# Performance work log

Hardware: AMD Instinct MI355X
Metric: run time of the kernel (lower is better)

The kernel has to match this reference:

```python
import jax, jax.numpy as jnp
import numpy as np

VOCAB, EMBED, ZCH = 4096, 128, 256
B, H, W = 32, 16, 16


def setup_inputs() -> dict:
    key = jax.random.key(0)
    k1, k2, k3, k4 = jax.random.split(key, 4)
    z_e = jax.random.normal(k1, (B, ZCH, H, W), dtype=jnp.float32)
    pre_w = jax.random.normal(k2, (EMBED, ZCH), dtype=jnp.float32) * 0.02
    pre_b = jnp.zeros((EMBED,), dtype=jnp.float32)
    # codebook initialized uniform(-1/vocab, 1/vocab) like the torch module
    emb = jax.random.uniform(k3, (VOCAB, EMBED), dtype=jnp.float32,
                             minval=-1.0 / VOCAB, maxval=1.0 / VOCAB)
    post_w = jax.random.normal(k4, (ZCH, EMBED), dtype=jnp.float32) * 0.02
    post_b = jnp.zeros((ZCH,), dtype=jnp.float32)
    return {"z_e": z_e, "pre_w": pre_w, "pre_b": pre_b, "emb": emb,
            "post_w": post_w, "post_b": post_b}


def reference(z_e, pre_w, pre_b, emb, post_w, post_b):
    # pre_quant_conv: 1x1 conv == per-pixel linear, z_channels -> embed_dim
    z = jnp.einsum('bchw,ec->behw', z_e, pre_w) + pre_b[None, :, None, None]
    b, e, h, w = z.shape
    zf = z.transpose(0, 2, 3, 1).reshape(-1, e)                 # (b*h*w, e)
    # squared distance to all codebook vectors: |z|^2 + |c|^2 - 2 z.c
    dist = (jnp.sum(zf * zf, axis=1, keepdims=True)
            + jnp.sum(emb * emb, axis=1)
            - 2.0 * zf @ emb.T)                                  # (b*h*w, vocab)
    tokens = jnp.argmin(dist, axis=-1)                           # (b*h*w,)
    z_q = emb[tokens].reshape(b, h, w, e).transpose(0, 3, 1, 2)  # (b,e,h,w)
    # straight-through estimator
    dec_in = z + jax.lax.stop_gradient(z_q - z)
    # post_quant_conv: 1x1 conv embed_dim -> z_channels (decoder input)
    rec = jnp.einsum('behw,ce->bchw', dec_in, post_w) + post_b[None, :, None, None]
    return z, z_q, rec
```

## Files before the change

kernel.cpp:

```cpp
#include <hip/hip_runtime.h>
#include <hip/hip_bf16.h>
#include <cstdint>

#define NB   32
#define NC   256
#define NE   128
#define NS   256
#define NV   4096
#define NP   8192
#define NSPLIT 8

typedef unsigned short ushort_t;
typedef __attribute__((ext_vector_type(8))) short bf16x8;
typedef __attribute__((ext_vector_type(8))) unsigned short us8;
typedef __attribute__((ext_vector_type(4))) float f32x4;

__device__ __forceinline__ float bf2f(ushort_t u) {
    union { unsigned int i; float f; } x; x.i = ((unsigned int)u) << 16; return x.f;
}
__device__ __forceinline__ ushort_t f2bf(float f) {
    __hip_bfloat16 h = __float2bfloat16(f);
    ushort_t u; __builtin_memcpy(&u, &h, 2); return u;
}
__device__ __forceinline__ unsigned asu(float f) { unsigned u; __builtin_memcpy(&u,&f,4); return u; }
__device__ __forceinline__ float    asf(unsigned u) { float f; __builtin_memcpy(&f,&u,4); return f; }

__global__ __launch_bounds__(256) void pre_conv_pack(
    const float* __restrict__ z_e, const float* __restrict__ pre_w,
    const float* __restrict__ pre_b, const float* __restrict__ emb,
    float* __restrict__ out_z, ushort_t* __restrict__ Bpack,
    float* __restrict__ cnorm)
{
    const int t = threadIdx.x;

    if (blockIdx.x == 8) {
        if (t < 128) {
            const int v = blockIdx.y * 128 + t;
            const float* row = emb + (size_t)v * NE;
            const int G = v >> 4;
            float nn = 0.f;
#pragma unroll
            for (int ks = 0; ks < 4; ks++) {
#pragma unroll
                for (int q = 0; q < 4; q++) {
                    us8 hv;
#pragma unroll
                    for (int j = 0; j < 8; j++) {
                        float x = row[ks * 32 + q * 8 + j];
                        nn = fmaf(x, x, nn);
                        hv[j] = f2bf(x);
                    }
                    const int L = (v & 15) | (q << 4);
                    *(us8*)(Bpack + ((size_t)G * 4 + ks) * 512 + L * 8) = hv;
                }
            }
            cnorm[v] = 0.5f * nn;
        }
        return;
    }

    const int e0 = blockIdx.x * 16;
    const int b  = blockIdx.y;
    const int s  = t;

    float acc[16];
#pragma unroll
    for (int r = 0; r < 16; r++) acc[r] = pre_b[e0 + r];

    const float* zin = z_e + (size_t)(b * NC) * NS + s;
    for (int c = 0; c < NC; c += 4) {
        float z0 = zin[(c + 0) * NS];
        float z1 = zin[(c + 1) * NS];
        float z2 = zin[(c + 2) * NS];
        float z3 = zin[(c + 3) * NS];
#pragma unroll
        for (int r = 0; r < 16; r++) {
            float4 w = *(const float4*)&pre_w[(e0 + r) * 256 + c];
            acc[r] = fmaf(z0, w.x, fmaf(z1, w.y, fmaf(z2, w.z, fmaf(z3, w.w, acc[r]))));
        }
    }
#pragma unroll
    for (int r = 0; r < 16; r++)
        out_z[(size_t)(b * NE + e0 + r) * NS + s] = acc[r];
}

__global__ __launch_bounds__(256, 3) void score_mfma(
    const float* __restrict__ z, const ushort_t* __restrict__ Bpack,
    const float* __restrict__ cnorm, int* __restrict__ pidx4)
{
    __shared__ __align__(16) char smraw[40960];
    float* As  = (float*)smraw;
    float* r1  = (float*)smraw;
    float* r2  = (float*)(smraw + 16640);
    float* t4b = (float*)(smraw + 33280);

    const int t = threadIdx.x;
    const int wave = t >> 6, lane = t & 63;
    const int set = blockIdx.x;
    const int split = blockIdx.y;
    const int p0 = set * 64;
    const int b  = p0 >> 8;
    const int s0 = p0 & 255;

    for (int idx = t; idx < 64 * 128; idx += 256) {
        int k = idx >> 6, i = idx & 63;
        As[i * 132 + k] = z[(size_t)(b * NE + k) * NS + s0 + i];
    }
    __syncthreads();

    const int am = lane & 15, aq = lane >> 4;
    bf16x8 ah[4][4];
#pragma unroll
    for (int mt = 0; mt < 4; mt++)
#pragma unroll
        for (int ks = 0; ks < 4; ks++) {
            const unsigned* src = (const unsigned*)(As + (mt * 16 + am) * 132 + ks * 32 + aq * 8);
            union { unsigned u[4]; bf16x8 v; } pk;
#pragma unroll
            for (int pr = 0; pr < 4; pr++)
                pk.u[pr] = (src[2 * pr + 1] & 0xFFFF0000u) | (src[2 * pr] >> 16);
            ah[mt][ks] = pk.v;
        }
    __syncthreads();

    const int Gbase = split * 32 + wave * 8;
    float cn[8];
#pragma unroll
    for (int cgi = 0; cgi < 8; cgi++)
        cn[cgi] = cnorm[(Gbase + cgi) * 16 + am];

    float b1v[16], b2v[16];
#pragma unroll
    for (int i = 0; i < 16; i++) { b1v[i] = -1e30f; b2v[i] = -1e30f; }

    bf16x8 bh[4], bhn[4];
#pragma unroll
    for (int ks = 0; ks < 4; ks++)
        bh[ks] = *(const bf16x8*)(Bpack + ((size_t)Gbase * 4 + ks) * 512 + lane * 8);

    for (int cgi = 0; cgi < 8; cgi++) {
        if (cgi < 7) {
#pragma unroll
            for (int ks = 0; ks < 4; ks++)
                bhn[ks] = *(const bf16x8*)(Bpack + ((size_t)(Gbase + cgi + 1) * 4 + ks) * 512 + lane * 8);
        }

        f32x4 acc[4];
#pragma unroll
        for (int mt = 0; mt < 4; mt++) acc[mt] = (f32x4){0.f, 0.f, 0.f, 0.f};
#pragma unroll
        for (int ks = 0; ks < 4; ks++)
#pragma unroll
            for (int mt = 0; mt < 4; mt++)
                acc[mt] = __builtin_amdgcn_mfma_f32_16x16x32_bf16(ah[mt][ks], bh[ks], acc[mt], 0, 0, 0);

#pragma unroll
        for (int mt = 0; mt < 4; mt++)
#pragma unroll
            for (int reg = 0; reg < 4; reg++) {
                const int si = mt * 4 + reg;
                float sc = acc[mt][reg] - cn[cgi];
                float ev = asf((asu(sc) & ~7u) | (unsigned)cgi);
                b2v[si] = fmaxf(b2v[si], fminf(ev, b1v[si]));
                b1v[si] = fmaxf(b1v[si], ev);
            }
#pragma unroll
        for (int ks = 0; ks < 4; ks++) bh[ks] = bhn[ks];
    }

    const int slot = wave * 16 + am;
#pragma unroll
    for (int mt = 0; mt < 4; mt++)
#pragma unroll
        for (int reg = 0; reg < 4; reg++) {
            int px = mt * 16 + aq * 4 + reg;
            r1[slot * 65 + px] = b1v[mt * 4 + reg];
            r2[slot * 65 + px] = b2v[mt * 4 + reg];
        }
    __syncthreads();

    {
        const int px = t >> 2, ch = t & 3;
        float t1 = -1e30f, t2 = -1e30f, t3 = -1e30f, t4 = -1e30f;
        for (int i = 0; i < 16; i++) {
            int sl = ch * 16 + i;
#pragma unroll
            for (int e = 0; e < 2; e++) {
                float raw = e ? r2[sl * 65 + px] : r1[sl * 65 + px];
                unsigned vb = asu(raw);
                float v = asf((vb & ~511u) | ((unsigned)sl << 3) | (vb & 7u));
                t4 = fmaxf(t4, fminf(v, t3));
                t3 = fmaxf(t3, fminf(v, t2));
                t2 = fmaxf(t2, fminf(v, t1));
                t1 = fmaxf(t1, v);
            }
        }
        float* dst = t4b + (px * 4 + ch) * 4;
        dst[0] = t1; dst[1] = t2; dst[2] = t3; dst[3] = t4;
    }
    __syncthreads();

    if (t < 64) {
        float u1 = -1e30f, u2 = -1e30f, u3 = -1e30f, u4 = -1e30f;
        for (int ch = 0; ch < 4; ch++) {
#pragma unroll
            for (int j = 0; j < 4; j++) {
                float v = t4b[(t * 4 + ch) * 4 + j];
                u4 = fmaxf(u4, fminf(v, u3));
                u3 = fmaxf(u3, fminf(v, u2));
                u2 = fmaxf(u2, fminf(v, u1));
                u1 = fmaxf(u1, v);
            }
        }
        const int p = p0 + t;
        float uu[4] = { u1, u2, u3, u4 };
#pragma unroll
        for (int j = 0; j < 4; j++) {
            unsigned bits = asu(uu[j]) & 511u;
            int w = (int)(bits >> 7), res = (int)((bits >> 3) & 15u), cg = (int)(bits & 7u);
            pidx4[((size_t)split * NP + p) * 4 + j] = split * 512 + (w * 8 + cg) * 16 + res;
        }
    }
}

__global__ __launch_bounds__(256) void rescore_gather(
    const float* __restrict__ z, const float* __restrict__ emb,
    const int* __restrict__ pidx4, float* __restrict__ out_zq)
{
    __shared__ __align__(16) float zl[32 * 132];
    __shared__ double bsl[32 * 8];
    __shared__ int    bil[32 * 8];
    __shared__ int    tok[32];

    const int t  = threadIdx.x;
    const int p0 = blockIdx.x * 32;
    const int b  = p0 >> 8;
    const int s0 = p0 & 255;

    for (int idx = t; idx < 32 * 128; idx += 256) {
        int k = idx >> 5, i = idx & 31;
        zl[i * 132 + k] = z[(size_t)(b * NE + k) * NS + s0 + i];
    }
    __syncthreads();

    const int il = t >> 3;
    const int ch = t & 7;
    const int p  = p0 + il;
    double bs = -1e300; int bi = 0x7fffffff;
#pragma unroll
    for (int j = 0; j < 4; j++) {
        int idx = pidx4[((size_t)ch * NP + p) * 4 + j];
        const float* er = emb + (size_t)idx * NE;
        double dot = 0.0, nn = 0.0;
        for (int k = 0; k < NE; k += 4) {
            float4 e4 = *(const float4*)(er + k);
            dot += (double)zl[il * 132 + k + 0] * (double)e4.x;
            dot += (double)zl[il * 132 + k + 1] * (double)e4.y;
            dot += (double)zl[il * 132 + k + 2] * (double)e4.z;
            dot += (double)zl[il * 132 + k + 3] * (double)e4.w;
            nn  += (double)e4.x * e4.x + (double)e4.y * e4.y
                 + (double)e4.z * e4.z + (double)e4.w * e4.w;
        }
        double sc = dot - 0.5 * nn;
        if (sc > bs || (sc == bs && idx < bi)) { bs = sc; bi = idx; }
    }
    bsl[il * 8 + ch] = bs;
    bil[il * 8 + ch] = bi;
    __syncthreads();

    if (t < 32) {
        double B = -1e300; int I = 0x7fffffff;
        for (int c = 0; c < 8; c++) {
            double sc = bsl[t * 8 + c]; int ii = bil[t * 8 + c];
            if (sc > B || (sc == B && ii < I)) { B = sc; I = ii; }
        }
        tok[t] = I;
    }
    __syncthreads();

    for (int idx = t; idx < NE * 32; idx += 256) {
        int e = idx >> 5, i = idx & 31;
        out_zq[(size_t)(b * NE + e) * NS + s0 + i] = emb[(size_t)tok[i] * NE + e];
    }
}

__global__ __launch_bounds__(256) void post_conv(
    const float* __restrict__ zq, const float* __restrict__ post_w,
    const float* __restrict__ post_b, float* __restrict__ out_rec)
{
    const int t  = threadIdx.x;
    const int c0 = blockIdx.x * 16;
    const int b  = blockIdx.y;
    const int s  = t;

    float acc[16];
#pragma unroll
    for (int r = 0; r < 16; r++) acc[r] = post_b[c0 + r];

    const float* zin = zq + (size_t)(b * NE) * NS + s;
    for (int e = 0; e < NE; e += 4) {
        float z0 = zin[(e + 0) * NS];
        float z1 = zin[(e + 1) * NS];
        float z2 = zin[(e + 2) * NS];
        float z3 = zin[(e + 3) * NS];
#pragma unroll
        for (int r = 0; r < 16; r++) {
            float4 w = *(const float4*)&post_w[(c0 + r) * 128 + e];
            acc[r] = fmaf(z0, w.x, fmaf(z1, w.y, fmaf(z2, w.z, fmaf(z3, w.w, acc[r]))));
        }
    }
#pragma unroll
    for (int r = 0; r < 16; r++)
        out_rec[(size_t)(b * NC + c0 + r) * NS + s] = acc[r];
}

extern "C" void kernel_launch(void* const* d_in, const int* in_sizes, int n_in,
                              void* d_out, int out_size, void* d_ws, size_t ws_size,
                              hipStream_t stream)
{
    const float* z_e    = (const float*)d_in[0];
    const float* pre_w  = (const float*)d_in[1];
    const float* pre_b  = (const float*)d_in[2];
    const float* emb    = (const float*)d_in[3];
    const float* post_w = (const float*)d_in[4];
    const float* post_b = (const float*)d_in[5];

    float* out     = (float*)d_out;
    float* out_z   = out;
    float* out_zq  = out + 1048576;
    float* out_rec = out + 2097152;

    const size_t SZ_BPACK = (size_t)256 * 4 * 512 * 2;
    const size_t SZ_CNORM = (size_t)NV * 4;
    const size_t SZ_PIDX4 = (size_t)NSPLIT * NP * 4 * 4;
    const size_t NEED = SZ_BPACK + SZ_CNORM + SZ_PIDX4;
    char* scr = (ws_size >= NEED) ? (char*)d_ws : (char*)out_rec;
    ushort_t* Bpack = (ushort_t*)scr;
    float*    cnorm = (float*)(scr + SZ_BPACK);
    int*      pidx4 = (int*)(scr + SZ_BPACK + SZ_CNORM);

    pre_conv_pack <<<dim3(9, 32),        256, 0, stream>>>(z_e, pre_w, pre_b, emb,
                                                           out_z, Bpack, cnorm);
    score_mfma    <<<dim3(128, NSPLIT),  256, 0, stream>>>(out_z, Bpack, cnorm, pidx4);
    rescore_gather<<<dim3(256),          256, 0, stream>>>(out_z, emb, pidx4, out_zq);
    post_conv     <<<dim3(16, 32),       256, 0, stream>>>(out_zq, post_w, post_b, out_rec);
}
```

Before: 177.5 us.

## Split-K conv kernels with LDS weight tiles and finer rescore/pack parallelism

The pre- and post-quant 1x1 conv kernels now stage a 16-row weight tile in LDS. They split the channel reduction across four waves and combine the partials through shared memory, and a new grid z dimension over spatial chunks gives four times more blocks. The codebook pack kernel now uses 8 threads per row with vector loads and a shuffle reduction for the norm. The rescore kernel handles 16 pixels per block with 16 threads per pixel, doubling its grid. The goal is to fix low occupancy and scalar weight loads from global memory, at the cost of extra LDS traffic and barriers.

```diff
diff --git a/kernel.cpp b/kernel.cpp
--- a/kernel.cpp
+++ b/kernel.cpp
@@ -31,57 +31,89 @@
     float* __restrict__ out_z, ushort_t* __restrict__ Bpack,
     float* __restrict__ cnorm)
 {
+    __shared__ __align__(16) float wtile[16 * 256];
+    __shared__ __align__(16) float part[4 * 16 * 64];
+
     const int t = threadIdx.x;
 
     if (blockIdx.x == 8) {
-        if (t < 128) {
-            const int v = blockIdx.y * 128 + t;
-            const float* row = emb + (size_t)v * NE;
-            const int G = v >> 4;
-            float nn = 0.f;
-#pragma unroll
-            for (int ks = 0; ks < 4; ks++) {
-#pragma unroll
-                for (int q = 0; q < 4; q++) {
-                    us8 hv;
-#pragma unroll
-                    for (int j = 0; j < 8; j++) {
-                        float x = row[ks * 32 + q * 8 + j];
-                        nn = fmaf(x, x, nn);
-                        hv[j] = f2bf(x);
-                    }
-                    const int L = (v & 15) | (q << 4);
-                    *(us8*)(Bpack + ((size_t)G * 4 + ks) * 512 + L * 8) = hv;
-                }
-            }
-            cnorm[v] = 0.5f * nn;
-        }
+        const int v     = (blockIdx.y * 4 + blockIdx.z) * 32 + (t >> 3);
+        const int chunk = t & 7;
+        const float4* rp = (const float4*)(emb + (size_t)v * NE + chunk * 16);
+        float4 x0 = rp[0], x1 = rp[1], x2 = rp[2], x3 = rp[3];
+        float xs[16] = { x0.x, x0.y, x0.z, x0.w, x1.x, x1.y, x1.z, x1.w,
+                         x2.x, x2.y, x2.z, x2.w, x3.x, x3.y, x3.z, x3.w };
+        us8 h0, h1;
+        float nn = 0.f;
+#pragma unroll
+        for (int j = 0; j < 8; j++) {
+            nn = fmaf(xs[j], xs[j], nn);
+            h0[j] = f2bf(xs[j]);
+        }
+#pragma unroll
+        for (int j = 0; j < 8; j++) {
+            nn = fmaf(xs[8 + j], xs[8 + j], nn);
+            h1[j] = f2bf(xs[8 + j]);
+        }
+        nn += __shfl_xor(nn, 1);
+        nn += __shfl_xor(nn, 2);
+        nn += __shfl_xor(nn, 4);
+        if (chunk == 0) cnorm[v] = 0.5f * nn;
+
+        const int G  = v >> 4;
+        const int ks = chunk >> 1;
+        const int q0 = (chunk & 1) * 2;
+        const int L0 = (v & 15) | (q0 << 4);
+        const int L1 = (v & 15) | ((q0 + 1) << 4);
+        *(us8*)(Bpack + ((size_t)G * 4 + ks) * 512 + L0 * 8) = h0;
+        *(us8*)(Bpack + ((size_t)G * 4 + ks) * 512 + L1 * 8) = h1;
         return;
     }
 
     const int e0 = blockIdx.x * 16;
     const int b  = blockIdx.y;
-    const int s  = t;
-
+    const int s0 = blockIdx.z * 64;
+
+    for (int idx = t; idx < 16 * 256; idx += 256)
+        wtile[idx] = pre_w[(e0 + (idx >> 8)) * 256 + (idx & 255)];
+    __syncthreads();
+
+    const int kq = t >> 6, sl = t & 63;
     float acc[16];
 #pragma unroll
-    for (int r = 0; r < 16; r++) acc[r] = pre_b[e0 + r];
-
-    const float* zin = z_e + (size_t)(b * NC) * NS + s;
-    for (int c = 0; c < NC; c += 4) {
+    for (int r = 0; r < 16; r++) acc[r] = 0.f;
+
+    const float* zin = z_e + (size_t)(b * NC + kq * 64) * NS + s0 + sl;
+    const int cb = kq * 64;
+#pragma unroll 4
+    for (int i = 0; i < 16; i++) {
+        const int c = i * 4;
         float z0 = zin[(c + 0) * NS];
         float z1 = zin[(c + 1) * NS];
         float z2 = zin[(c + 2) * NS];
         float z3 = zin[(c + 3) * NS];
 #pragma unroll
         for (int r = 0; r < 16; r++) {
-            float4 w = *(const float4*)&pre_w[(e0 + r) * 256 + c];
+            float4 w = *(const float4*)&wtile[r * 256 + cb + c];
             acc[r] = fmaf(z0, w.x, fmaf(z1, w.y, fmaf(z2, w.z, fmaf(z3, w.w, acc[r]))));
         }
     }
 #pragma unroll
     for (int r = 0; r < 16; r++)
-        out_z[(size_t)(b * NE + e0 + r) * NS + s] = acc[r];
+        part[(kq * 16 + r) * 64 + sl] = acc[r];
+    __syncthreads();
+
+    const int r4 = t >> 6, sl2 = t & 63;
+#pragma unroll
+    for (int j = 0; j < 4; j++) {
+        const int r = j * 4 + r4;
+        float v = pre_b[e0 + r]
+                + part[(0 * 16 + r) * 64 + sl2]
+                + part[(1 * 16 + r) * 64 + sl2]
+                + part[(2 * 16 + r) * 64 + sl2]
+                + part[(3 * 16 + r) * 64 + sl2];
+        out_z[(size_t)(b * NE + e0 + r) * NS + s0 + sl2] = v;
+    }
 }
 
 __global__ __launch_bounds__(256, 3) void score_mfma(
@@ -227,29 +259,31 @@
     const float* __restrict__ z, const float* __restrict__ emb,
     const int* __restrict__ pidx4, float* __restrict__ out_zq)
 {
-    __shared__ __align__(16) float zl[32 * 132];
-    __shared__ double bsl[32 * 8];
-    __shared__ int    bil[32 * 8];
-    __shared__ int    tok[32];
+    __shared__ __align__(16) float zl[16 * 132];
+    __shared__ double bsl[16 * 16];
+    __shared__ int    bil[16 * 16];
+    __shared__ int    tok[16];
 
     const int t  = threadIdx.x;
-    const int p0 = blockIdx.x * 32;
+    const int p0 = blockIdx.x * 16;
     const int b  = p0 >> 8;
     const int s0 = p0 & 255;
 
-    for (int idx = t; idx < 32 * 128; idx += 256) {
-        int k = idx >> 5, i = idx & 31;
+    for (int idx = t; idx < 16 * 128; idx += 256) {
+        int k = idx >> 4, i = idx & 15;
         zl[i * 132 + k] = z[(size_t)(b * NE + k) * NS + s0 + i];
     }
     __syncthreads();
 
-    const int il = t >> 3;
-    const int ch = t & 7;
+    const int il = t >> 4;
+    const int cc = t & 15;
     const int p  = p0 + il;
     double bs = -1e300; int bi = 0x7fffffff;
 #pragma unroll
-    for (int j = 0; j < 4; j++) {
-        int idx = pidx4[((size_t)ch * NP + p) * 4 + j];
+    for (int jj = 0; jj < 2; jj++) {
+        int cand = cc * 2 + jj;
+        int split = cand >> 2, slot = cand & 3;
+        int idx = pidx4[((size_t)split * NP + p) * 4 + slot];
         const float* er = emb + (size_t)idx * NE;
         double dot = 0.0, nn = 0.0;
         for (int k = 0; k < NE; k += 4) {
@@ -264,22 +298,22 @@
         double sc = dot - 0.5 * nn;
         if (sc > bs || (sc == bs && idx < bi)) { bs = sc; bi = idx; }
     }
-    bsl[il * 8 + ch] = bs;
-    bil[il * 8 + ch] = bi;
-    __syncthreads();
-
-    if (t < 32) {
+    bsl[il * 16 + cc] = bs;
+    bil[il * 16 + cc] = bi;
+    __syncthreads();
+
+    if (t < 16) {
         double B = -1e300; int I = 0x7fffffff;
-        for (int c = 0; c < 8; c++) {
-            double sc = bsl[t * 8 + c]; int ii = bil[t * 8 + c];
+        for (int c = 0; c < 16; c++) {
+            double sc = bsl[t * 16 + c]; int ii = bil[t * 16 + c];
             if (sc > B || (sc == B && ii < I)) { B = sc; I = ii; }
         }
         tok[t] = I;
     }
     __syncthreads();
 
-    for (int idx = t; idx < NE * 32; idx += 256) {
-        int e = idx >> 5, i = idx & 31;
+    for (int idx = t; idx < NE * 16; idx += 256) {
+        int e = idx >> 4, i = idx & 15;
         out_zq[(size_t)(b * NE + e) * NS + s0 + i] = emb[(size_t)tok[i] * NE + e];
     }
 }
@@ -288,30 +322,54 @@
     const float* __restrict__ zq, const float* __restrict__ post_w,
     const float* __restrict__ post_b, float* __restrict__ out_rec)
 {
+    __shared__ __align__(16) float wtile[16 * 128];
+    __shared__ __align__(16) float part[4 * 16 * 64];
+
     const int t  = threadIdx.x;
     const int c0 = blockIdx.x * 16;
     const int b  = blockIdx.y;
-    const int s  = t;
-
+    const int s0 = blockIdx.z * 64;
+
+    for (int idx = t; idx < 16 * 128; idx += 256)
+        wtile[idx] = post_w[(c0 + (idx >> 7)) * 128 + (idx & 127)];
+    __syncthreads();
+
+    const int kq = t >> 6, sl = t & 63;
     float acc[16];
 #pragma unroll
-    for (int r = 0; r < 16; r++) acc[r] = post_b[c0 + r];
-
-    const float* zin = zq + (size_t)(b * NE) * NS + s;
-    for (int e = 0; e < NE; e += 4) {
+    for (int r = 0; r < 16; r++) acc[r] = 0.f;
+
+    const float* zin = zq + (size_t)(b * NE + kq * 32) * NS + s0 + sl;
+    const int eb = kq * 32;
+#pragma unroll 4
+    for (int i = 0; i < 8; i++) {
+        const int e = i * 4;
         float z0 = zin[(e + 0) * NS];
         float z1 = zin[(e + 1) * NS];
         float z2 = zin[(e + 2) * NS];
         float z3 = zin[(e + 3) * NS];
 #pragma unroll
         for (int r = 0; r < 16; r++) {
-            float4 w = *(const float4*)&post_w[(c0 + r) * 128 + e];
+            float4 w = *(const float4*)&wtile[r * 128 + eb + e];
             acc[r] = fmaf(z0, w.x, fmaf(z1, w.y, fmaf(z2, w.z, fmaf(z3, w.w, acc[r]))));
         }
     }
 #pragma unroll
     for (int r = 0; r < 16; r++)
-        out_rec[(size_t)(b * NC + c0 + r) * NS + s] = acc[r];
+        part[(kq * 16 + r) * 64 + sl] = acc[r];
+    __syncthreads();
+
+    const int r4 = t >> 6, sl2 = t & 63;
+#pragma unroll
+    for (int j = 0; j < 4; j++) {
+        const int r = j * 4 + r4;
+        float v = post_b[c0 + r]
+                + part[(0 * 16 + r) * 64 + sl2]
+                + part[(1 * 16 + r) * 64 + sl2]
+                + part[(2 * 16 + r) * 64 + sl2]
+                + part[(3 * 16 + r) * 64 + sl2];
+        out_rec[(size_t)(b * NC + c0 + r) * NS + s0 + sl2] = v;
+    }
 }
 
 extern "C" void kernel_launch(void* const* d_in, const int* in_sizes, int n_in,
@@ -339,9 +397,9 @@
     float*    cnorm = (float*)(scr + SZ_BPACK);
     int*      pidx4 = (int*)(scr + SZ_BPACK + SZ_CNORM);
 
-    pre_conv_pack <<<dim3(9, 32),        256, 0, stream>>>(z_e, pre_w, pre_b, emb,
+    pre_conv_pack <<<dim3(9, 32, 4),     256, 0, stream>>>(z_e, pre_w, pre_b, emb,
                                                            out_z, Bpack, cnorm);
     score_mfma    <<<dim3(128, NSPLIT),  256, 0, stream>>>(out_z, Bpack, cnorm, pidx4);
-    rescore_gather<<<dim3(256),          256, 0, stream>>>(out_z, emb, pidx4, out_zq);
-    post_conv     <<<dim3(16, 32),       256, 0, stream>>>(out_zq, post_w, post_b, out_rec);
-}
+    rescore_gather<<<dim3(512),          256, 0, stream>>>(out_z, emb, pidx4, out_zq);
+    post_conv     <<<dim3(16, 32, 4),    256, 0, stream>>>(out_zq, post_w, post_b, out_rec);
+}
```

Result: faster. 152.5 us (-14.1%).
